# Performance work log

Hardware: AMD Instinct MI355X
Metric: run time of the kernel (lower is better)

Reference implementation:

```python
import jax, jax.numpy as jnp
import numpy as np

B, CIN, COUT, H, W, K = 32, 256, 256, 56, 56, 3
STRIDE, PAD, DIL = 1, 1, 1
SPARSITY = 0.9  # fraction of weight entries pruned to zero


def setup_inputs() -> dict:
    key = jax.random.key(0)
    kx, kw, km = jax.random.split(key, 3)
    x = jax.random.normal(kx, (B, CIN, H, W), dtype=jnp.float32)
    w = jax.random.normal(kw, (COUT, CIN, K, K), dtype=jnp.float32)
    mask = (jax.random.uniform(km, (COUT, CIN, K, K)) > SPARSITY).astype(jnp.float32)
    w = w * mask
    return {"x": x, "weight": w}


def reference(x, weight):
    # Faithful math of SparseConv2D.forward (sparse path == nn.Conv2d, bias=None):
    # NCHW input, OIHW weight, stride/pad/dilation as configured.
    out = jax.lax.conv_general_dilated(
        x, weight,
        window_strides=(STRIDE, STRIDE),
        padding=[(PAD, PAD), (PAD, PAD)],
        rhs_dilation=(DIL, DIL),
        dimension_numbers=("NCHW", "OIHW", "NCHW"),
    )
    return out  # [B, COUT, H_out, W_out]
```

## Files before the change

kernel.cpp:

```cpp
#include <hip/hip_runtime.h>


typedef __attribute__((ext_vector_type(8))) short short8;
typedef __attribute__((ext_vector_type(4))) float f32x4;
typedef __attribute__((ext_vector_type(4))) int i32x4;

constexpr int BB = 32, CIN = 256, COUT = 256, H = 56, W = 56, HW = H * W;
constexpr int HP = 58, WP = 58;

constexpr size_t XP_ELEMS = (size_t)BB * HP * WP * CIN;
constexpr size_t WB_ELEMS = (size_t)COUT * 9 * CIN;
constexpr size_t WS_NEEDED = (XP_ELEMS + WB_ELEMS) * 2;

__device__ __forceinline__ ushort f2bf(float f) {
    unsigned x = __float_as_uint(f);
    unsigned r = (x + 0x7FFFu + ((x >> 16) & 1u)) >> 16;
    return (ushort)r;
}


__global__ __launch_bounds__(256)
void prep_xp(const float* __restrict__ x, ushort* __restrict__ xp) {
    const int bi = blockIdx.x;
    const int b = bi / HP, i = bi % HP;
    ushort* dst = xp + (size_t)bi * WP * CIN;
    const int tid = threadIdx.x;

    if (i == 0 || i == HP - 1) {
        i32x4 z = {0, 0, 0, 0};
        for (int k = tid; k < WP * CIN / 8; k += 256) ((i32x4*)dst)[k] = z;
        return;
    }

    __shared__ ushort t[W][CIN + 2];
    const int lane = tid & 63, wv = tid >> 6;
    if (lane < W) {
        const float* src = x + (size_t)b * CIN * HW + (size_t)(i - 1) * W + lane;
        for (int cin = wv; cin < CIN; cin += 4)
            t[lane][cin] = f2bf(src[(size_t)cin * HW]);
    }
    __syncthreads();
    for (int c = 0; c < WP; ++c)
        dst[c * CIN + tid] = (c == 0 || c == WP - 1) ? (ushort)0 : t[c - 1][tid];
}

__global__ __launch_bounds__(256)
void prep_wb2(const float* __restrict__ w, ushort* __restrict__ wb2) {
    const int d = blockIdx.x * 256 + threadIdx.x;
    const int ci = d & 31;
    const int cout = (d >> 5) & 255;
    const int r = d >> 13;
    const int tap = r % 9, cb = r / 9;
    const int cin = cb * 32 + ci;
    wb2[d] = f2bf(w[((size_t)cout * CIN + cin) * 9 + tap]);
}


#define SCHED_FENCE() __builtin_amdgcn_sched_barrier(0)
#define WAITV(N) asm volatile("s_waitcnt vmcnt(" #N ")" ::: "memory")

__device__ __forceinline__ void gload_lds16(const ushort* g, ushort* l) {
    __builtin_amdgcn_global_load_lds(
        (const __attribute__((address_space(1))) void*)g,
        (__attribute__((address_space(3))) void*)l, 16, 0, 0);
}

__device__ __forceinline__ int swz(int c) { return c ^ ((c >> 3) & 7); }

__global__ __launch_bounds__(256, 3)
void conv_mfma(const ushort* __restrict__ xp, const ushort* __restrict__ wb2,
               float* __restrict__ out) {
    int bx = blockIdx.x;
    bx = (bx & 7) * 224 + (bx >> 3);

    const int mt = bx & 1;
    const int nt = bx >> 1;
    const int b  = nt / 28;
    const int p0 = (nt % 28) * 112;
    const int r0 = p0 / 56;

    const int tid  = threadIdx.x;
    const int wv   = tid >> 6;
    const int lane = tid & 63;
    const int ml   = lane & 15;
    const int g    = lane >> 4;

    __shared__ ushort As0[2 * 4096], As1[2 * 4096];
    __shared__ ushort Xs[4 * 2048];

    int aoffB[2];
    #pragma unroll
    for (int mi = 0; mi < 2; ++mi)
        aoffB[mi] = swz((32 * wv + 16 * mi + ml) * 4 + g) * 16;
    int cbase[7];
    #pragma unroll
    for (int nf = 0; nf < 7; ++nf) {
        const int p_  = p0 + 16 * nf + ml;
        const int hl  = (p_ >= p0 + 56) ? 1 : 0;
        const int col = p_ - 56 * (r0 + hl);
        cbase[nf] = hl * 256 + col * 4 + g;
    }
    int goffA[2];
    #pragma unroll
    for (int k = 0; k < 2; ++k) {
        const int c = swz(k * 256 + tid);
        goffA[k] = (c >> 2) * 32 + (c & 3) * 8;
    }
    int xoff;
    {
        const int ii = (tid & 0xC0) | ((tid & 63) ^ (((tid & 63) >> 3) & 7));
        xoff = (ii < 232) ? ((ii >> 2) * CIN + (ii & 3) * 8) : 0;
    }
    const size_t xbase = ((size_t)b * HP + r0) * WP * CIN;
    const ushort* wbase = wb2 + mt * 4096;

    f32x4 acc[2][7] = {};

    #define STAGE_A2(S, BUF)                                                    \
        { _Pragma("unroll")                                                     \
          for (int s = 0; s < 2; ++s) {                                         \
              int _sl = (S) + s; if (_sl >= 72) _sl -= 72;                      \
              const ushort* _src = wbase + (size_t)_sl * 8192;                  \
              _Pragma("unroll")                                                 \
              for (int k = 0; k < 2; ++k)                                       \
                  gload_lds16(_src + goffA[k],                                  \
                              (BUF) + s * 4096 + (k * 256 + wv * 64) * 8);      \
          } }
    #define STAGE_A1(S, BUF)                                                    \
        { int _sl = (S); if (_sl >= 72) _sl -= 72;                              \
          const ushort* _src = wbase + (size_t)_sl * 8192;                      \
          _Pragma("unroll")                                                     \
          for (int k = 0; k < 2; ++k)                                           \
              gload_lds16(_src + goffA[k], (BUF) + (k * 256 + wv * 64) * 8); }
    #define STAGE_XPAIR(RR, CBN)                                                \
        { _Pragma("unroll")                                                     \
          for (int r_ = 0; r_ < 2; ++r_)                                        \
              gload_lds16(xp + xbase + (size_t)((RR) + r_) * WP * CIN           \
                              + (CBN) * 32 + xoff,                              \
                          &Xs[(((RR) + r_) * 256 + wv * 64) * 8]); }

    STAGE_XPAIR(0, 0);
    STAGE_XPAIR(2, 0);
    STAGE_A2(0, As0);
    STAGE_A2(2, As1);
    WAITV(0);
    __syncthreads();

    #define PHASE(CB, Q, NTAPS, HWAIT)                                          \
        {                                                                       \
            WAITV(HWAIT);                                                       \
            SCHED_FENCE();                                                      \
            __builtin_amdgcn_s_barrier();                                       \
            SCHED_FENCE();                                                      \
            const ushort* Ab = (((CB) + (Q)) & 1) ? As1 : As0;                  \
            _Pragma("unroll")                                                   \
            for (int tp = 0; tp < (NTAPS); ++tp) {                              \
                const int tap = 2 * (Q) + tp;                                   \
                const int kh = tap / 3, kw = tap - kh * 3;                      \
                short8 av[2], bv[7];                                            \
                _Pragma("unroll")                                               \
                for (int mi = 0; mi < 2; ++mi)                                  \
                    av[mi] = *(const short8*)((const char*)Ab + tp * 8192       \
                                              + aoffB[mi]);                     \
                _Pragma("unroll")                                               \
                for (int nf = 0; nf < 7; ++nf) {                                \
                    const int c = cbase[nf] + kh * 256 + kw * 4;                \
                    bv[nf] = *(const short8*)((const char*)Xs + swz(c) * 16);   \
                }                                                               \
                __builtin_amdgcn_s_setprio(1);                                  \
                _Pragma("unroll")                                               \
                for (int mi = 0; mi < 2; ++mi)                                  \
                    _Pragma("unroll")                                           \
                    for (int nf = 0; nf < 7; ++nf)                              \
                        acc[mi][nf] = __builtin_amdgcn_mfma_f32_16x16x32_bf16(  \
                                          av[mi], bv[nf], acc[mi][nf], 0, 0, 0);\
                __builtin_amdgcn_s_setprio(0);                                  \
            }                                                                   \
            SCHED_FENCE();                                                      \
            __builtin_amdgcn_s_barrier();                                       \
            SCHED_FENCE();                                                      \
        }

    for (int cbp = 0; cbp < 4; ++cbp) {
        #pragma unroll
        for (int hf = 0; hf < 2; ++hf) {
            const int cb  = 2 * cbp + hf;
            const int t0  = 9 * cb;
            const int cbn = (cb < 7) ? cb + 1 : 0;
            ushort* bufE = ((cb & 1) == 0) ? As0 : As1;
            ushort* bufO = ((cb & 1) == 0) ? As1 : As0;

            PHASE(cb, 0, 2, 6);
            STAGE_A2(t0 + 4, bufE);
            SCHED_FENCE();
            PHASE(cb, 1, 2, 4);
            STAGE_A2(t0 + 6, bufO);
            SCHED_FENCE();
            PHASE(cb, 2, 2, 4);
            STAGE_XPAIR(0, cbn);
            STAGE_A1(t0 + 8, bufE);
            SCHED_FENCE();
            PHASE(cb, 3, 2, 4);
            STAGE_A2(t0 + 9, bufO);
            SCHED_FENCE();
            PHASE(cb, 4, 1, 4);
            STAGE_XPAIR(2, cbn);
            STAGE_A2(t0 + 11, bufE);
            SCHED_FENCE();
        }
    }
    WAITV(0);

    float* ob = out + (size_t)b * COUT * HW;
    #pragma unroll
    for (int mi = 0; mi < 2; ++mi)
        #pragma unroll
        for (int nf = 0; nf < 7; ++nf)
            #pragma unroll
            for (int r = 0; r < 4; ++r) {
                const int cout_l = mt * 128 + 32 * wv + 16 * mi + 4 * g + r;
                const int p_ = p0 + 16 * nf + ml;
                ob[(size_t)cout_l * HW + p_] = acc[mi][nf][r];
            }
    #undef STAGE_A2
    #undef STAGE_A1
    #undef STAGE_XPAIR
    #undef PHASE
}


constexpr int WSZ = CIN * 9;
constexpr int NIN = 54 * 54;

__global__ __launch_bounds__(256)
void sparse_conv3x3(const float* __restrict__ x,
                    const float* __restrict__ wgt,
                    float* __restrict__ out) {
    const int bc = blockIdx.x, cout = bc % COUT, b = bc / COUT;
    const int tid = threadIdx.x;
    __shared__ int2 s_ent[WSZ];
    __shared__ unsigned char s_kk[WSZ];
    __shared__ int s_cnt[257];
    const float* wc = wgt + (size_t)cout * WSZ;
    float mv[9]; int cnt = 0;
    #pragma unroll
    for (int i = 0; i < 9; ++i) { mv[i] = wc[tid * 9 + i]; if (mv[i] != 0.0f) cnt++; }
    s_cnt[tid] = cnt; __syncthreads();
    if (tid == 0) { int run = 0; for (int t = 0; t < 256; ++t) { int c = s_cnt[t]; s_cnt[t] = run; run += c; } s_cnt[256] = run; }
    __syncthreads();
    { int pos = s_cnt[tid];
      #pragma unroll
      for (int i = 0; i < 9; ++i) if (mv[i] != 0.0f) {
          const int kh = i / 3, kw = i - kh * 3;
          int2 e; e.x = (tid * HW + (kh - 1) * W + (kw - 1)) * 4; e.y = __float_as_int(mv[i]);
          s_ent[pos] = e; s_kk[pos] = (unsigned char)(kh | (kw << 4)); pos++; } }
    __syncthreads();
    const int nnz = s_cnt[256];
    const char* xb = (const char*)(x + (size_t)b * CIN * HW);
    float* ob = out + (size_t)bc * HW;
    for (int o = tid; o < HW; o += 256) {
        int h, w; bool interior = (o < NIN);
        if (interior) { h = 1 + o / 54; w = 1 + (o - (h - 1) * 54); }
        else { int o2 = o - NIN;
            if (o2 < 56) { h = 0; w = o2; } else if (o2 < 112) { h = 55; w = o2 - 56; }
            else if (o2 < 166) { h = 1 + (o2 - 112); w = 0; } else { h = 1 + (o2 - 166); w = 55; } }
        const char* pb = xb + (size_t)(h * W + w) * 4;
        float acc = 0.0f;
        if (interior) {
            #pragma unroll 4
            for (int e = 0; e < nnz; ++e) { const int2 en = s_ent[e];
                acc = fmaf(__int_as_float(en.y), *(const float*)(pb + en.x), acc); }
        } else {
            const int h1 = h - 1, w1 = w - 1;
            for (int e = 0; e < nnz; ++e) { const int2 en = s_ent[e]; const int kk = s_kk[e];
                const int hh = h1 + (kk & 15), ww = w1 + (kk >> 4);
                if ((unsigned)hh < (unsigned)H && (unsigned)ww < (unsigned)W)
                    acc = fmaf(__int_as_float(en.y), *(const float*)(pb + en.x), acc); } }
        ob[h * W + w] = acc;
    }
}


extern "C" void kernel_launch(void* const* d_in, const int* in_sizes, int n_in,
                              void* d_out, int out_size, void* d_ws, size_t ws_size,
                              hipStream_t stream) {
    const float* x = (const float*)d_in[0];
    const float* w = (const float*)d_in[1];
    float* out = (float*)d_out;

    if (ws_size >= WS_NEEDED) {
        ushort* xp = (ushort*)d_ws;
        ushort* wbp = xp + XP_ELEMS;
        prep_xp<<<BB * HP, 256, 0, stream>>>(x, xp);
        prep_wb2<<<(int)(WB_ELEMS / 256), 256, 0, stream>>>(w, wbp);
        conv_mfma<<<1792, 256, 0, stream>>>(xp, wbp, out);
    } else {
        sparse_conv3x3<<<BB * COUT, 256, 0, stream>>>(x, w, out);
    }
}
```

Before: 143.6 us.

## Load weight fragments directly from global into registers instead of staging through LDS

Removes the LDS double buffers for the weight (A) operand. Each wave now loads its MFMA A fragments straight from global memory into register double buffers (aA/aB), issued after each phase's MFMAs so they overlap the next phase. This cuts LDS traffic and footprint, which may allow higher occupancy. In exchange, every wave issues its own uncoalesced 16-byte global loads that rely on L2/L1 hits, and the new loads share the vmcnt wait counter with the X staging loads, which the wait counts may not match.

```diff
diff --git a/kernel.cpp b/kernel.cpp
--- a/kernel.cpp
+++ b/kernel.cpp
@@ -85,13 +85,8 @@
     const int ml   = lane & 15;
     const int g    = lane >> 4;
 
-    __shared__ ushort As0[2 * 4096], As1[2 * 4096];
     __shared__ ushort Xs[4 * 2048];
 
-    int aoffB[2];
-    #pragma unroll
-    for (int mi = 0; mi < 2; ++mi)
-        aoffB[mi] = swz((32 * wv + 16 * mi + ml) * 4 + g) * 16;
     int cbase[7];
     #pragma unroll
     for (int nf = 0; nf < 7; ++nf) {
@@ -100,68 +95,51 @@
         const int col = p_ - 56 * (r0 + hl);
         cbase[nf] = hl * 256 + col * 4 + g;
     }
-    int goffA[2];
-    #pragma unroll
-    for (int k = 0; k < 2; ++k) {
-        const int c = swz(k * 256 + tid);
-        goffA[k] = (c >> 2) * 32 + (c & 3) * 8;
-    }
+    int afo[2];
+    #pragma unroll
+    for (int mi = 0; mi < 2; ++mi)
+        afo[mi] = (mt * 128 + 32 * wv + 16 * mi + ml) * 32 + 8 * g;
     int xoff;
     {
         const int ii = (tid & 0xC0) | ((tid & 63) ^ (((tid & 63) >> 3) & 7));
         xoff = (ii < 232) ? ((ii >> 2) * CIN + (ii & 3) * 8) : 0;
     }
     const size_t xbase = ((size_t)b * HP + r0) * WP * CIN;
-    const ushort* wbase = wb2 + mt * 4096;
 
     f32x4 acc[2][7] = {};
-
-    #define STAGE_A2(S, BUF)                                                    \
-        { _Pragma("unroll")                                                     \
-          for (int s = 0; s < 2; ++s) {                                         \
-              int _sl = (S) + s; if (_sl >= 72) _sl -= 72;                      \
-              const ushort* _src = wbase + (size_t)_sl * 8192;                  \
-              _Pragma("unroll")                                                 \
-              for (int k = 0; k < 2; ++k)                                       \
-                  gload_lds16(_src + goffA[k],                                  \
-                              (BUF) + s * 4096 + (k * 256 + wv * 64) * 8);      \
-          } }
-    #define STAGE_A1(S, BUF)                                                    \
-        { int _sl = (S); if (_sl >= 72) _sl -= 72;                              \
-          const ushort* _src = wbase + (size_t)_sl * 8192;                      \
-          _Pragma("unroll")                                                     \
-          for (int k = 0; k < 2; ++k)                                           \
-              gload_lds16(_src + goffA[k], (BUF) + (k * 256 + wv * 64) * 8); }
+    short8 aA[2][2], aB[2][2];
+
     #define STAGE_XPAIR(RR, CBN)                                                \
         { _Pragma("unroll")                                                     \
           for (int r_ = 0; r_ < 2; ++r_)                                        \
               gload_lds16(xp + xbase + (size_t)((RR) + r_) * WP * CIN           \
                               + (CBN) * 32 + xoff,                              \
                           &Xs[(((RR) + r_) * 256 + wv * 64) * 8]); }
-
-    STAGE_XPAIR(0, 0);
-    STAGE_XPAIR(2, 0);
-    STAGE_A2(0, As0);
-    STAGE_A2(2, As1);
-    WAITV(0);
-    __syncthreads();
-
-    #define PHASE(CB, Q, NTAPS, HWAIT)                                          \
+    #define LOADA2(BUF, T)                                                      \
+        { _Pragma("unroll")                                                     \
+          for (int tp = 0; tp < 2; ++tp) {                                      \
+              int _t = (T) + tp; if (_t >= 72) _t -= 72;                        \
+              const ushort* _s = wb2 + (size_t)_t * 8192;                       \
+              BUF[tp][0] = *(const short8*)(_s + afo[0]);                       \
+              BUF[tp][1] = *(const short8*)(_s + afo[1]);                       \
+          } }
+    #define LOADA1(BUF, T)                                                      \
+        { int _t = (T); if (_t >= 72) _t -= 72;                                 \
+          const ushort* _s = wb2 + (size_t)_t * 8192;                           \
+          BUF[0][0] = *(const short8*)(_s + afo[0]);                            \
+          BUF[0][1] = *(const short8*)(_s + afo[1]); }
+
+    #define PHASE(BUF, T0, NTAPS, HWAIT, LOADNEXT)                              \
         {                                                                       \
             WAITV(HWAIT);                                                       \
             SCHED_FENCE();                                                      \
             __builtin_amdgcn_s_barrier();                                       \
             SCHED_FENCE();                                                      \
-            const ushort* Ab = (((CB) + (Q)) & 1) ? As1 : As0;                  \
             _Pragma("unroll")                                                   \
             for (int tp = 0; tp < (NTAPS); ++tp) {                              \
-                const int tap = 2 * (Q) + tp;                                   \
+                const int tap = (T0) % 9 + tp;                                  \
                 const int kh = tap / 3, kw = tap - kh * 3;                      \
-                short8 av[2], bv[7];                                            \
-                _Pragma("unroll")                                               \
-                for (int mi = 0; mi < 2; ++mi)                                  \
-                    av[mi] = *(const short8*)((const char*)Ab + tp * 8192       \
-                                              + aoffB[mi]);                     \
+                short8 bv[7];                                                   \
                 _Pragma("unroll")                                               \
                 for (int nf = 0; nf < 7; ++nf) {                                \
                     const int c = cbase[nf] + kh * 256 + kw * 4;                \
@@ -173,13 +151,22 @@
                     _Pragma("unroll")                                           \
                     for (int nf = 0; nf < 7; ++nf)                              \
                         acc[mi][nf] = __builtin_amdgcn_mfma_f32_16x16x32_bf16(  \
-                                          av[mi], bv[nf], acc[mi][nf], 0, 0, 0);\
+                                          BUF[tp][mi], bv[nf], acc[mi][nf],     \
+                                          0, 0, 0);                             \
                 __builtin_amdgcn_s_setprio(0);                                  \
             }                                                                   \
+            LOADNEXT;                       \
             SCHED_FENCE();                                                      \
             __builtin_amdgcn_s_barrier();                                       \
             SCHED_FENCE();                                                      \
         }
+
+    STAGE_XPAIR(0, 0);
+    STAGE_XPAIR(2, 0);
+    LOADA2(aA, 0);
+    LOADA2(aB, 2);
+    WAITV(0);
+    __syncthreads();
 
     for (int cbp = 0; cbp < 4; ++cbp) {
         #pragma unroll
@@ -187,26 +174,27 @@
             const int cb  = 2 * cbp + hf;
             const int t0  = 9 * cb;
             const int cbn = (cb < 7) ? cb + 1 : 0;
-            ushort* bufE = ((cb & 1) == 0) ? As0 : As1;
-            ushort* bufO = ((cb & 1) == 0) ? As1 : As0;
-
-            PHASE(cb, 0, 2, 6);
-            STAGE_A2(t0 + 4, bufE);
-            SCHED_FENCE();
-            PHASE(cb, 1, 2, 4);
-            STAGE_A2(t0 + 6, bufO);
-            SCHED_FENCE();
-            PHASE(cb, 2, 2, 4);
-            STAGE_XPAIR(0, cbn);
-            STAGE_A1(t0 + 8, bufE);
-            SCHED_FENCE();
-            PHASE(cb, 3, 2, 4);
-            STAGE_A2(t0 + 9, bufO);
-            SCHED_FENCE();
-            PHASE(cb, 4, 1, 4);
-            STAGE_XPAIR(2, cbn);
-            STAGE_A2(t0 + 11, bufE);
-            SCHED_FENCE();
+            if (hf == 0) {
+                PHASE(aA, t0 + 0, 2, 6, LOADA2(aA, t0 + 4));
+                PHASE(aB, t0 + 2, 2, 4, LOADA2(aB, t0 + 6));
+                PHASE(aA, t0 + 4, 2, 4, LOADA1(aA, t0 + 8));
+                STAGE_XPAIR(0, cbn);
+                SCHED_FENCE();
+                PHASE(aB, t0 + 6, 2, 4, LOADA2(aB, t0 + 9));
+                PHASE(aA, t0 + 8, 1, 6, LOADA2(aA, t0 + 11));
+                STAGE_XPAIR(2, cbn);
+                SCHED_FENCE();
+            } else {
+                PHASE(aB, t0 + 0, 2, 6, LOADA2(aB, t0 + 4));
+                PHASE(aA, t0 + 2, 2, 4, LOADA2(aA, t0 + 6));
+                PHASE(aB, t0 + 4, 2, 4, LOADA1(aB, t0 + 8));
+                STAGE_XPAIR(0, cbn);
+                SCHED_FENCE();
+                PHASE(aA, t0 + 6, 2, 4, LOADA2(aA, t0 + 9));
+                PHASE(aB, t0 + 8, 1, 6, LOADA2(aB, t0 + 11));
+                STAGE_XPAIR(2, cbn);
+                SCHED_FENCE();
+            }
         }
     }
     WAITV(0);
@@ -222,9 +210,9 @@
                 const int p_ = p0 + 16 * nf + ml;
                 ob[(size_t)cout_l * HW + p_] = acc[mi][nf][r];
             }
-    #undef STAGE_A2
-    #undef STAGE_A1
     #undef STAGE_XPAIR
+    #undef LOADA2
+    #undef LOADA1
     #undef PHASE
 }
 
```

Result: slower. 247.8 us (+72.5%).
